# Kernel optimization log

Hardware: AMD Instinct MI355X
Metric: run time of the kernel (lower is better)

Reference implementation:

```python
import jax, jax.numpy as jnp
import numpy as np

N, E = 50000, 400000
IN_DIM = OUT_DIM = 128
T, R, H = 4, 8, 8
DK = OUT_DIM // H


def setup_inputs() -> dict:
    key = jax.random.key(0)
    ks = jax.random.split(key, 20)
    xav = lambda k, i, o: jax.random.uniform(k, (T, i, o), jnp.float32, -1.0, 1.0) * np.sqrt(6.0 / (i + o))
    return {
        "node_inp": jax.random.normal(ks[0], (N, IN_DIM), jnp.float32),
        "node_type": jax.random.randint(ks[1], (N,), 0, T),
        "edge_index": jax.random.randint(ks[2], (2, E), 0, N),
        "edge_type": jax.random.randint(ks[3], (E,), 0, R),
        "edge_sign": jax.random.randint(ks[4], (E,), 0, 3) - 1,  # values in {-1,0,1}
        "Wq": xav(ks[5], IN_DIM, OUT_DIM), "bq": jnp.zeros((T, OUT_DIM)),
        "Wk": xav(ks[6], IN_DIM, OUT_DIM), "bk": jnp.zeros((T, OUT_DIM)),
        "Wv": xav(ks[7], IN_DIM, OUT_DIM), "bv": jnp.zeros((T, OUT_DIM)),
        "rel_q": jax.random.normal(ks[8], (R, H, DK), jnp.float32),
        "rel_k": jax.random.normal(ks[9], (R, H, DK), jnp.float32),
        "rel_v": jax.random.normal(ks[10], (R, H, DK), jnp.float32),
        "sign_k_neutral": jnp.ones((H, DK), jnp.float32),
        "sign_v_neutral": jnp.ones((H, DK), jnp.float32),
        "rel_bias": jnp.zeros((R, H), jnp.float32),
        "skip": jnp.ones((T,), jnp.float32),
        "ln_gamma": jnp.ones((T, OUT_DIM), jnp.float32),
        "ln_beta": jnp.zeros((T, OUT_DIM), jnp.float32),
    }


def reference(node_inp, node_type, edge_index, edge_type, edge_sign,
              Wq, bq, Wk, bk, Wv, bv, rel_q, rel_k, rel_v,
              sign_k_neutral, sign_v_neutral, rel_bias, skip, ln_gamma, ln_beta):
    n = node_inp.shape[0]
    src, dst = edge_index[0], edge_index[1]
    rows = jnp.arange(n)
    # per-node-type linear projections: compute for all types, select by node_type
    proj = lambda W, b: (jnp.einsum('ni,tio->tno', node_inp, W) + b[:, None, :])[node_type, rows]
    Q = proj(Wq, bq).reshape(n, H, DK)
    K = proj(Wk, bk).reshape(n, H, DK)
    V = proj(Wv, bv).reshape(n, H, DK)
    # sign tables: [neg(-1), pos(+1), neutral]
    ones = jnp.ones((H, DK), node_inp.dtype)
    sign_k_all = jnp.stack([-ones, ones, sign_k_neutral], 0)
    sign_v_all = jnp.stack([-ones, ones, sign_v_neutral], 0)
    s_idx = jnp.where(edge_sign == -1, 0, jnp.where(edge_sign == 1, 1, 2))
    q_eff = Q[dst] * rel_q[edge_type]                      # [E,H,DK]
    k_eff = K[src] * rel_k[edge_type] * sign_k_all[s_idx]
    v_eff = V[src] * rel_v[edge_type] * sign_v_all[s_idx]
    scores = (q_eff * k_eff).sum(-1) / np.sqrt(DK) + rel_bias[edge_type]  # [E,H]
    # segment softmax over dst groups
    smax = jax.ops.segment_max(scores, dst, num_segments=n)
    ex = jnp.exp(scores - smax[dst])
    ssum = jax.ops.segment_sum(ex, dst, num_segments=n)
    attn = ex / (ssum[dst] + 1e-16)
    msg = (v_eff * attn[..., None]).reshape(-1, OUT_DIM)
    out = jnp.zeros((n, OUT_DIM), node_inp.dtype).at[dst].add(msg)
    # per-type gated skip + layernorm
    alpha = jax.nn.sigmoid(skip)[node_type][:, None]
    pre = alpha * out + (1.0 - alpha) * node_inp
    mu = pre.mean(-1, keepdims=True)
    var = ((pre - mu) ** 2).mean(-1, keepdims=True)
    normed = (pre - mu) / jnp.sqrt(var + 1e-5)
    return normed * ln_gamma[node_type] + ln_beta[node_type]
```

## Files before the change

### kernel.cpp

```cpp
#include <hip/hip_runtime.h>
#include <hip/hip_bf16.h>


#define D 128
#define NT 4
#define NR 8
#define NH 8
#define SCAN_BS 256

typedef unsigned short ushort_t;
typedef unsigned int uint_t;
typedef __attribute__((ext_vector_type(8))) short short8v;
typedef __attribute__((ext_vector_type(4))) float f32x4;

static __device__ __forceinline__ ushort_t f2bf(float f) {
    uint_t u = __float_as_uint(f);
    return (ushort_t)((u + 0x7FFFu + ((u >> 16) & 1u)) >> 16);
}
static __device__ __forceinline__ float bf2f(ushort_t h) {
    return __uint_as_float(((uint_t)h) << 16);
}

__global__ void k_hist(const int* __restrict__ nt, const int* __restrict__ ei,
                       int N, int E, int* __restrict__ tcnt, int* __restrict__ deg) {
    __shared__ int lcnt[NT];
    int tid = threadIdx.x;
    if (tid < NT) lcnt[tid] = 0;
    __syncthreads();
    int g = blockIdx.x * 256 + tid;
    if (g < N) atomicAdd(&lcnt[nt[g]], 1);
    if (g < E) atomicAdd(&deg[ei[E + g]], 1);
    __syncthreads();
    if (tid < NT && lcnt[tid]) atomicAdd(&tcnt[tid], lcnt[tid]);
}

__global__ __launch_bounds__(SCAN_BS) void k_scan1(const int* __restrict__ deg, int N,
                                                   int* __restrict__ bsum) {
    __shared__ int lds[SCAN_BS];
    int ti = threadIdx.x;
    int i = blockIdx.x * SCAN_BS + ti;
    lds[ti] = (i < N) ? deg[i] : 0;
    __syncthreads();
    for (int off = SCAN_BS >> 1; off > 0; off >>= 1) {
        if (ti < off) lds[ti] += lds[ti + off];
        __syncthreads();
    }
    if (ti == 0) bsum[blockIdx.x] = lds[0];
}

__global__ __launch_bounds__(SCAN_BS) void k_scan2(const int* __restrict__ bsum, int NB,
                                                   const int* __restrict__ tcnt,
                                                   int* __restrict__ bbase,
                                                   int* __restrict__ toff,
                                                   int* __restrict__ row_ptr, int N, int E) {
    __shared__ int lds[SCAN_BS];
    int ti = threadIdx.x;
    int v = (ti < NB) ? bsum[ti] : 0;
    lds[ti] = v;
    __syncthreads();
    for (int off = 1; off < SCAN_BS; off <<= 1) {
        int t = (ti >= off) ? lds[ti - off] : 0;
        __syncthreads();
        lds[ti] += t;
        __syncthreads();
    }
    if (ti < NB) bbase[ti] = lds[ti] - v;
    if (ti == 0) {
        int a = 0;
        for (int t = 0; t < NT; t++) { toff[t] = a; a += tcnt[t]; }
        toff[NT] = a;
        row_ptr[N] = E;
    }
}

__global__ __launch_bounds__(SCAN_BS) void k_scan3(const int* __restrict__ deg, int N,
                                                   const int* __restrict__ bbase,
                                                   int* __restrict__ row_ptr,
                                                   int* __restrict__ ecur) {
    __shared__ int lds[SCAN_BS];
    int ti = threadIdx.x;
    int i = blockIdx.x * SCAN_BS + ti;
    int v = (i < N) ? deg[i] : 0;
    lds[ti] = v;
    __syncthreads();
    for (int off = 1; off < SCAN_BS; off <<= 1) {
        int t = (ti >= off) ? lds[ti - off] : 0;
        __syncthreads();
        lds[ti] += t;
        __syncthreads();
    }
    if (i < N) {
        int ex = bbase[blockIdx.x] + lds[ti] - v;
        row_ptr[i] = ex;
        ecur[i] = ex;
    }
}

__global__ void k_scatter(const int* __restrict__ nt, const int* __restrict__ ei,
                          const int* __restrict__ et, const int* __restrict__ es,
                          int N, int E, int* __restrict__ tcur,
                          const int* __restrict__ toff, int* __restrict__ sorted,
                          int* __restrict__ ecur, int* __restrict__ csr_rec) {
    __shared__ int lcnt[NT];
    __shared__ int lbase[NT];
    int tid = threadIdx.x;
    if (tid < NT) lcnt[tid] = 0;
    __syncthreads();
    int g = blockIdx.x * 256 + tid;
    int t = -1, myrank = 0;
    if (g < N) {
        t = nt[g];
        myrank = atomicAdd(&lcnt[t], 1);
    }
    __syncthreads();
    if (tid < NT) lbase[tid] = lcnt[tid] ? atomicAdd(&tcur[tid], lcnt[tid]) : 0;
    __syncthreads();
    if (t >= 0) sorted[toff[t] + lbase[t] + myrank] = g;

    if (g < E) {
        int src = ei[g];
        int d = ei[E + g];
        int r = et[g];
        int sg = es[g];
        int p = atomicAdd(&ecur[d], 1);
        csr_rec[p] = src | (r << 17) | ((sg + 1) << 20);
    }
}

__global__ void k_wprep(const float* __restrict__ Wq, const float* __restrict__ Wk,
                        const float* __restrict__ Wv,
                        ushort_t* __restrict__ wt_hi, ushort_t* __restrict__ wt_lo) {
    int g = blockIdx.x * 256 + threadIdx.x;
    if (g >= 3 * NT * D * D) return;
    int o = g & 127;
    int k = (g >> 7) & 127;
    int t = (g >> 14) & 3;
    int m = g >> 16;
    const float* Wsel = (m == 0) ? Wq : (m == 1) ? Wk : Wv;
    float w = Wsel[((size_t)t * D + k) * D + o];
    ushort_t hi = f2bf(w);
    ushort_t lo = f2bf(w - bf2f(hi));
    size_t dst = (((size_t)(m * NT + t) * D) + o) * D + k;
    wt_hi[dst] = hi;
    wt_lo[dst] = lo;
}

__global__ void k_xprep(const float* __restrict__ x, const int* __restrict__ sorted,
                        int N, ushort_t* __restrict__ xs_hi, ushort_t* __restrict__ xs_lo) {
    int g = blockIdx.x * 256 + threadIdx.x;
    if (g >= N * 32) return;
    int i = g >> 5;
    int c4 = (g & 31) * 4;
    int node = sorted[i];
    float4 v = *(const float4*)(x + (size_t)node * D + c4);
    ushort4 h, l;
    h.x = f2bf(v.x); l.x = f2bf(v.x - bf2f(h.x));
    h.y = f2bf(v.y); l.y = f2bf(v.y - bf2f(h.y));
    h.z = f2bf(v.z); l.z = f2bf(v.z - bf2f(h.z));
    h.w = f2bf(v.w); l.w = f2bf(v.w - bf2f(h.w));
    *(ushort4*)(xs_hi + (size_t)i * D + c4) = h;
    *(ushort4*)(xs_lo + (size_t)i * D + c4) = l;
}

__global__ __launch_bounds__(512) void k_projm(
    const ushort_t* __restrict__ xs_hi, const ushort_t* __restrict__ xs_lo,
    const ushort_t* __restrict__ wt_hi, const ushort_t* __restrict__ wt_lo,
    const int* __restrict__ sorted, const int* __restrict__ toff,
    const float* __restrict__ bq, const float* __restrict__ bk,
    const float* __restrict__ bv,
    float* __restrict__ Q, ushort_t* __restrict__ Kb, ushort_t* __restrict__ Vb) {
    __shared__ int sid[128];
    int tid = threadIdx.x;
    int b = blockIdx.x;
    int t = -1, p0 = 0;
    int cum = 0;
    for (int tt = 0; tt < NT; tt++) {
        int cnt_t = toff[tt + 1] - toff[tt];
        int nb = (cnt_t + 127) >> 7;
        if (t < 0 && b < cum + nb) { t = tt; p0 = toff[tt] + (b - cum) * 128; }
        cum += nb;
    }
    if (t < 0) return;
    int tend = toff[t + 1];
    if (tid < 128) sid[tid] = (p0 + tid < tend) ? sorted[p0 + tid] : -1;
    __syncthreads();

    int w = tid >> 6, lane = tid & 63;
    int wr = w >> 2, wc = w & 3;
    int l15 = lane & 15, kq = lane >> 4;
    int m = blockIdx.y;

    const ushort_t* wth = wt_hi + ((size_t)(m * NT + t) * D) * D;
    const ushort_t* wtl = wt_lo + ((size_t)(m * NT + t) * D) * D;

    f32x4 acc[4][2];
#pragma unroll
    for (int fa = 0; fa < 4; fa++)
#pragma unroll
        for (int fb = 0; fb < 2; fb++) acc[fa][fb] = 0.f;

#pragma unroll
    for (int k0 = 0; k0 < D; k0 += 32) {
        int kk = k0 + kq * 8;
        short8v ah[4], al[4];
#pragma unroll
        for (int fa = 0; fa < 4; fa++) {
            size_t row = (size_t)(p0 + wr * 64 + fa * 16 + l15);
            ah[fa] = *(const short8v*)(xs_hi + row * D + kk);
            al[fa] = *(const short8v*)(xs_lo + row * D + kk);
        }
        short8v bh[2], bl[2];
#pragma unroll
        for (int fb = 0; fb < 2; fb++) {
            size_t col = (size_t)(wc * 32 + fb * 16 + l15);
            bh[fb] = *(const short8v*)(wth + col * D + kk);
            bl[fb] = *(const short8v*)(wtl + col * D + kk);
        }
#pragma unroll
        for (int fa = 0; fa < 4; fa++)
#pragma unroll
            for (int fb = 0; fb < 2; fb++) {
                acc[fa][fb] = __builtin_amdgcn_mfma_f32_16x16x32_bf16(
                    al[fa], bh[fb], acc[fa][fb], 0, 0, 0);
                acc[fa][fb] = __builtin_amdgcn_mfma_f32_16x16x32_bf16(
                    ah[fa], bl[fb], acc[fa][fb], 0, 0, 0);
                acc[fa][fb] = __builtin_amdgcn_mfma_f32_16x16x32_bf16(
                    ah[fa], bh[fb], acc[fa][fb], 0, 0, 0);
            }
    }

    const float* bm = (m == 0) ? bq : (m == 1) ? bk : bv;
    bm += t * D;
    float bias0 = bm[wc * 32 + l15];
    float bias1 = bm[wc * 32 + 16 + l15];
#pragma unroll
    for (int fa = 0; fa < 4; fa++) {
#pragma unroll
        for (int reg = 0; reg < 4; reg++) {
            int local = wr * 64 + fa * 16 + kq * 4 + reg;
            int node = sid[local];
            if (node < 0) continue;
            float v0 = acc[fa][0][reg] + bias0;
            float v1 = acc[fa][1][reg] + bias1;
            int col0 = wc * 32 + l15;
            if (m == 0) {
                Q[(size_t)node * D + col0] = v0;
                Q[(size_t)node * D + col0 + 16] = v1;
            } else {
                ushort_t* Om = (m == 1) ? Kb : Vb;
                Om[(size_t)node * D + col0] = f2bf(v0);
                Om[(size_t)node * D + col0 + 16] = f2bf(v1);
            }
        }
    }
}

__global__ __launch_bounds__(256) void k_agg(
    const int* __restrict__ row_ptr, const int* __restrict__ csr_rec,
    const int* __restrict__ nt, const float* __restrict__ x,
    const float* __restrict__ Qt, const ushort_t* __restrict__ Kb,
    const ushort_t* __restrict__ Vb, const float* __restrict__ rq,
    const float* __restrict__ rk, const float* __restrict__ rv,
    const float* __restrict__ skn, const float* __restrict__ svn,
    const float* __restrict__ rb, const float* __restrict__ skip,
    const float* __restrict__ gamma, const float* __restrict__ beta,
    float* __restrict__ out, int N) {
    __shared__ float l_rq[NR * 132];
    __shared__ float l_rk[NR * 132];
    __shared__ float l_rv[NR * 132];
    __shared__ float l_rb[NR * NH];
    int tid = threadIdx.x;
    for (int idx = tid; idx < NR * D; idx += 256) {
        int r = idx >> 7, c = idx & 127;
        l_rq[r * 132 + c] = rq[idx];
        l_rk[r * 132 + c] = rk[idx];
        l_rv[r * 132 + c] = rv[idx];
    }
    if (tid < NR * NH) l_rb[tid] = rb[tid];
    __syncthreads();

    int wid = (blockIdx.x * 256 + tid) >> 6;
    if (wid >= N) return;
    int lane = tid & 63;
    int h = lane >> 3, li = lane & 7;
    int d0 = lane * 2;
    int dst = wid;
    int rp0 = row_ptr[dst];
    int deg = row_ptr[dst + 1] - rp0;

    float4 q4[4], sk4[4];
#pragma unroll
    for (int j = 0; j < 4; j++) {
        q4[j] = *(const float4*)(Qt + (size_t)dst * D + h * 16 + 4 * j);
        sk4[j] = *(const float4*)(skn + h * 16 + 4 * j);
    }
    float2 sv2 = *(const float2*)(svn + d0);
    float2 xi = *(const float2*)(x + (size_t)dst * D + d0);
    int t = nt[dst];

    float m = -INFINITY, lsum = 0.f, acc0 = 0.f, acc1 = 0.f;

    for (int c0 = 0; c0 < deg; c0 += 8) {
        int cn = min(8, deg - c0);
        bool valid = li < cn;
        int recA = csr_rec[rp0 + c0 + (valid ? li : 0)];
        int srcA = recA & 0x1FFFF;
        int rA = (recA >> 17) & 7;
        int sgA = ((recA >> 20) & 3) - 1;
        bool neuA = (sgA == 0);
        float fsgA = (float)sgA;
        const ushort_t* kp = Kb + (size_t)srcA * D + h * 16;
        const float* rqp = &l_rq[rA * 132 + h * 16];
        const float* rkp = &l_rk[rA * 132 + h * 16];
        float dot = 0.f;
#pragma unroll
        for (int j = 0; j < 4; j++) {
            ushort4 kk = ((const ushort4*)kp)[j];
            float k0 = bf2f(kk.x), k1 = bf2f(kk.y), k2 = bf2f(kk.z), k3 = bf2f(kk.w);
            float4 a4 = *(const float4*)(rqp + 4 * j);
            float4 b4 = *(const float4*)(rkp + 4 * j);
            float f0 = neuA ? sk4[j].x : fsgA;
            float f1 = neuA ? sk4[j].y : fsgA;
            float f2 = neuA ? sk4[j].z : fsgA;
            float f3 = neuA ? sk4[j].w : fsgA;
            dot += q4[j].x * a4.x * k0 * b4.x * f0;
            dot += q4[j].y * a4.y * k1 * b4.y * f1;
            dot += q4[j].z * a4.z * k2 * b4.z * f2;
            dot += q4[j].w * a4.w * k3 * b4.w * f3;
        }
        float scA = valid ? dot * 0.25f + l_rb[rA * NH + h] : -INFINITY;
        float cm = scA;
        cm = fmaxf(cm, __shfl_xor(cm, 1));
        cm = fmaxf(cm, __shfl_xor(cm, 2));
        cm = fmaxf(cm, __shfl_xor(cm, 4));
        float nm = fmaxf(m, cm);
        float resc = __expf(m - nm);
        acc0 *= resc; acc1 *= resc; lsum *= resc;
        m = nm;
        int rec_[8];
        float w_[8];
        uint_t v2_[8];
#pragma unroll
        for (int i = 0; i < 8; i++) {
            rec_[i] = __shfl(recA, i);
            int src = rec_[i] & 0x1FFFF;
            v2_[i] = *(const uint_t*)(Vb + (size_t)src * D + d0);
            float s = __shfl(scA, (lane & 56) | i);
            w_[i] = __expf(s - m);
        }
#pragma unroll
        for (int i = 0; i < 8; i++) {
            float w = w_[i];
            lsum += w;
            int r = (rec_[i] >> 17) & 7;
            int sg = ((rec_[i] >> 20) & 3) - 1;
            float v0 = bf2f((ushort_t)(v2_[i] & 0xFFFF));
            float v1 = bf2f((ushort_t)(v2_[i] >> 16));
            float2 r2 = *(const float2*)(&l_rv[r * 132 + d0]);
            bool neu = (sg == 0);
            float f0 = neu ? sv2.x : (float)sg;
            float f1 = neu ? sv2.y : (float)sg;
            acc0 += w * v0 * r2.x * f0;
            acc1 += w * v1 * r2.y * f1;
        }
    }
    float winv = 1.f / (lsum + 1e-16f);
    float a0 = acc0 * winv, a1 = acc1 * winv;

    float alpha = 1.f / (1.f + __expf(-skip[t]));
    float p0 = alpha * a0 + (1.f - alpha) * xi.x;
    float p1 = alpha * a1 + (1.f - alpha) * xi.y;
    float rs = p0 + p1, rsq = p0 * p0 + p1 * p1;
#pragma unroll
    for (int o = 1; o < 64; o <<= 1) {
        rs += __shfl_xor(rs, o);
        rsq += __shfl_xor(rsq, o);
    }
    float mu = rs * (1.f / 128.f);
    float var = rsq * (1.f / 128.f) - mu * mu;
    float rstd = rsqrtf(var + 1e-5f);
    float2 g2 = *(const float2*)(gamma + t * D + d0);
    float2 b2 = *(const float2*)(beta + t * D + d0);
    float o0 = (p0 - mu) * rstd * g2.x + b2.x;
    float o1 = (p1 - mu) * rstd * g2.y + b2.y;
    *(float2*)(out + (size_t)dst * D + d0) = make_float2(o0, o1);
}

extern "C" void kernel_launch(void* const* d_in, const int* in_sizes, int n_in,
                              void* d_out, int out_size, void* d_ws, size_t ws_size,
                              hipStream_t stream) {
    const float* x   = (const float*)d_in[0];
    const int*  nt   = (const int*)d_in[1];
    const int*  ei   = (const int*)d_in[2];
    const int*  et   = (const int*)d_in[3];
    const int*  es   = (const int*)d_in[4];
    const float* Wq  = (const float*)d_in[5];
    const float* bq  = (const float*)d_in[6];
    const float* Wk  = (const float*)d_in[7];
    const float* bk  = (const float*)d_in[8];
    const float* Wv  = (const float*)d_in[9];
    const float* bv  = (const float*)d_in[10];
    const float* rq  = (const float*)d_in[11];
    const float* rk  = (const float*)d_in[12];
    const float* rv  = (const float*)d_in[13];
    const float* skn = (const float*)d_in[14];
    const float* svn = (const float*)d_in[15];
    const float* rb  = (const float*)d_in[16];
    const float* skp = (const float*)d_in[17];
    const float* gma = (const float*)d_in[18];
    const float* bta = (const float*)d_in[19];
    float* out = (float*)d_out;

    int N = in_sizes[0] / D;
    int E = in_sizes[2] / 2;
    int NB = (N + SCAN_BS - 1) / SCAN_BS;

    float*    Q     = (float*)d_ws;
    ushort_t* Kb    = (ushort_t*)(Q + (size_t)N * D);
    ushort_t* Vb    = Kb + (size_t)N * D;
    ushort_t* xs_hi = Vb + (size_t)N * D;
    ushort_t* xs_lo = xs_hi + (size_t)N * D;
    ushort_t* wt_hi = xs_lo + (size_t)N * D;
    ushort_t* wt_lo = wt_hi + (size_t)3 * NT * D * D;
    int* deg     = (int*)(wt_lo + (size_t)3 * NT * D * D);
    int* tcnt    = deg + N;
    int* tcur    = tcnt + NT;
    int* row_ptr = tcur + NT;
    int* ecur    = row_ptr + N + 1;
    int* toff    = ecur + N;
    int* sorted  = toff + 8;
    int* csr_rec = sorted + N;
    int* bsum    = csr_rec + E;
    int* bbase   = bsum + NB;

    hipMemsetAsync(deg, 0, (size_t)(N + 2 * NT) * sizeof(int), stream);

    int gbNE = (max(N, E) + 255) / 256;
    k_wprep<<<(3 * NT * D * D + 255) / 256, 256, 0, stream>>>(Wq, Wk, Wv, wt_hi, wt_lo);
    k_hist<<<gbNE, 256, 0, stream>>>(nt, ei, N, E, tcnt, deg);
    k_scan1<<<NB, SCAN_BS, 0, stream>>>(deg, N, bsum);
    k_scan2<<<1, SCAN_BS, 0, stream>>>(bsum, NB, tcnt, bbase, toff, row_ptr, N, E);
    k_scan3<<<NB, SCAN_BS, 0, stream>>>(deg, N, bbase, row_ptr, ecur);
    k_scatter<<<gbNE, 256, 0, stream>>>(nt, ei, et, es, N, E, tcur, toff, sorted,
                                        ecur, csr_rec);
    k_xprep<<<(N * 32 + 255) / 256, 256, 0, stream>>>(x, sorted, N, xs_hi, xs_lo);
    int nbp = (N + 127) / 128 + NT;
    k_projm<<<dim3(nbp, 3), 512, 0, stream>>>(xs_hi, xs_lo, wt_hi, wt_lo, sorted,
                                              toff, bq, bk, bv, Q, Kb, Vb);
    k_agg<<<(N * 64 + 255) / 256, 256, 0, stream>>>(row_ptr, csr_rec, nt, x, Q, Kb, Vb,
                                                    rq, rk, rv, skn, svn, rb, skp,
                                                    gma, bta, out, N);
}
```

Baseline: 330.1 us.

## Make aggregation kernel persistent with grid-stride waves and wider K loads

The aggregation kernel now launches a fixed grid of 2048 blocks in which each wave loops over destination nodes with a grid stride. The per-block LDS setup of relation tables is therefore amortised over many nodes instead of repeated in 12500 blocks. K rows are read as two 16-byte loads instead of four 8-byte ones, and each lane computes its own exponential once before it is shuffled, rather than every lane recomputing eight. A fixed grid can leave load imbalanced across waves when node degrees vary.

```diff
diff --git a/kernel.cpp b/kernel.cpp
--- a/kernel.cpp
+++ b/kernel.cpp
@@ -19,6 +19,12 @@
 }
 static __device__ __forceinline__ float bf2f(ushort_t h) {
     return __uint_as_float(((uint_t)h) << 16);
+}
+static __device__ __forceinline__ float bflo(uint_t u) {
+    return __uint_as_float(u << 16);
+}
+static __device__ __forceinline__ float bfhi(uint_t u) {
+    return __uint_as_float(u & 0xFFFF0000u);
 }
 
 __global__ void k_hist(const int* __restrict__ nt, const int* __restrict__ ei,
@@ -279,111 +285,123 @@
     if (tid < NR * NH) l_rb[tid] = rb[tid];
     __syncthreads();
 
-    int wid = (blockIdx.x * 256 + tid) >> 6;
-    if (wid >= N) return;
     int lane = tid & 63;
     int h = lane >> 3, li = lane & 7;
     int d0 = lane * 2;
-    int dst = wid;
-    int rp0 = row_ptr[dst];
-    int deg = row_ptr[dst + 1] - rp0;
-
-    float4 q4[4], sk4[4];
-#pragma unroll
-    for (int j = 0; j < 4; j++) {
-        q4[j] = *(const float4*)(Qt + (size_t)dst * D + h * 16 + 4 * j);
-        sk4[j] = *(const float4*)(skn + h * 16 + 4 * j);
-    }
+
+    float4 sk4[4];
+#pragma unroll
+    for (int j = 0; j < 4; j++) sk4[j] = *(const float4*)(skn + h * 16 + 4 * j);
     float2 sv2 = *(const float2*)(svn + d0);
-    float2 xi = *(const float2*)(x + (size_t)dst * D + d0);
-    int t = nt[dst];
-
-    float m = -INFINITY, lsum = 0.f, acc0 = 0.f, acc1 = 0.f;
-
-    for (int c0 = 0; c0 < deg; c0 += 8) {
-        int cn = min(8, deg - c0);
-        bool valid = li < cn;
-        int recA = csr_rec[rp0 + c0 + (valid ? li : 0)];
-        int srcA = recA & 0x1FFFF;
-        int rA = (recA >> 17) & 7;
-        int sgA = ((recA >> 20) & 3) - 1;
-        bool neuA = (sgA == 0);
-        float fsgA = (float)sgA;
-        const ushort_t* kp = Kb + (size_t)srcA * D + h * 16;
-        const float* rqp = &l_rq[rA * 132 + h * 16];
-        const float* rkp = &l_rk[rA * 132 + h * 16];
-        float dot = 0.f;
-#pragma unroll
-        for (int j = 0; j < 4; j++) {
-            ushort4 kk = ((const ushort4*)kp)[j];
-            float k0 = bf2f(kk.x), k1 = bf2f(kk.y), k2 = bf2f(kk.z), k3 = bf2f(kk.w);
-            float4 a4 = *(const float4*)(rqp + 4 * j);
-            float4 b4 = *(const float4*)(rkp + 4 * j);
-            float f0 = neuA ? sk4[j].x : fsgA;
-            float f1 = neuA ? sk4[j].y : fsgA;
-            float f2 = neuA ? sk4[j].z : fsgA;
-            float f3 = neuA ? sk4[j].w : fsgA;
-            dot += q4[j].x * a4.x * k0 * b4.x * f0;
-            dot += q4[j].y * a4.y * k1 * b4.y * f1;
-            dot += q4[j].z * a4.z * k2 * b4.z * f2;
-            dot += q4[j].w * a4.w * k3 * b4.w * f3;
+
+    int wid0 = (blockIdx.x * 256 + tid) >> 6;
+    int wstride = (gridDim.x * 256) >> 6;
+
+    for (int dst = wid0; dst < N; dst += wstride) {
+        int rp0 = row_ptr[dst];
+        int deg = row_ptr[dst + 1] - rp0;
+        float4 q4[4];
+#pragma unroll
+        for (int j = 0; j < 4; j++)
+            q4[j] = *(const float4*)(Qt + (size_t)dst * D + h * 16 + 4 * j);
+        float2 xi = *(const float2*)(x + (size_t)dst * D + d0);
+        int t = nt[dst];
+
+        float m = -INFINITY, lsum = 0.f, acc0 = 0.f, acc1 = 0.f;
+
+        for (int c0 = 0; c0 < deg; c0 += 8) {
+            int cn = min(8, deg - c0);
+            bool valid = li < cn;
+            int recA = csr_rec[rp0 + c0 + (valid ? li : 0)];
+            int srcA = recA & 0x1FFFF;
+            int rA = (recA >> 17) & 7;
+            int sgA = ((recA >> 20) & 3) - 1;
+            bool neuA = (sgA == 0);
+            float fsgA = (float)sgA;
+            const uint4* kp4 = (const uint4*)(Kb + (size_t)srcA * D + h * 16);
+            uint4 kA = kp4[0], kB = kp4[1];
+            float ke[16];
+            ke[0] = bflo(kA.x); ke[1] = bfhi(kA.x);
+            ke[2] = bflo(kA.y); ke[3] = bfhi(kA.y);
+            ke[4] = bflo(kA.z); ke[5] = bfhi(kA.z);
+            ke[6] = bflo(kA.w); ke[7] = bfhi(kA.w);
+            ke[8] = bflo(kB.x); ke[9] = bfhi(kB.x);
+            ke[10] = bflo(kB.y); ke[11] = bfhi(kB.y);
+            ke[12] = bflo(kB.z); ke[13] = bfhi(kB.z);
+            ke[14] = bflo(kB.w); ke[15] = bfhi(kB.w);
+            const float* rqp = &l_rq[rA * 132 + h * 16];
+            const float* rkp = &l_rk[rA * 132 + h * 16];
+            float dot = 0.f;
+#pragma unroll
+            for (int j = 0; j < 4; j++) {
+                float4 a4 = *(const float4*)(rqp + 4 * j);
+                float4 b4 = *(const float4*)(rkp + 4 * j);
+                float f0 = neuA ? sk4[j].x : fsgA;
+                float f1 = neuA ? sk4[j].y : fsgA;
+                float f2 = neuA ? sk4[j].z : fsgA;
+                float f3 = neuA ? sk4[j].w : fsgA;
+                dot += q4[j].x * a4.x * ke[4 * j] * b4.x * f0;
+                dot += q4[j].y * a4.y * ke[4 * j + 1] * b4.y * f1;
+                dot += q4[j].z * a4.z * ke[4 * j + 2] * b4.z * f2;
+                dot += q4[j].w * a4.w * ke[4 * j + 3] * b4.w * f3;
+            }
+            float scA = valid ? dot * 0.25f + l_rb[rA * NH + h] : -INFINITY;
+            float cm = scA;
+            cm = fmaxf(cm, __shfl_xor(cm, 1));
+            cm = fmaxf(cm, __shfl_xor(cm, 2));
+            cm = fmaxf(cm, __shfl_xor(cm, 4));
+            float nm = fmaxf(m, cm);
+            float resc = __expf(m - nm);
+            acc0 *= resc; acc1 *= resc; lsum *= resc;
+            m = nm;
+            float expA = __expf(scA - m);
+            int rec_[8];
+            float w_[8];
+            uint_t v2_[8];
+#pragma unroll
+            for (int i = 0; i < 8; i++) {
+                rec_[i] = __shfl(recA, i);
+                int src = rec_[i] & 0x1FFFF;
+                v2_[i] = *(const uint_t*)(Vb + (size_t)src * D + d0);
+                w_[i] = __shfl(expA, (lane & 56) | i);
+            }
+#pragma unroll
+            for (int i = 0; i < 8; i++) {
+                float w = w_[i];
+                lsum += w;
+                int r = (rec_[i] >> 17) & 7;
+                int sg = ((rec_[i] >> 20) & 3) - 1;
+                float v0 = bflo(v2_[i]);
+                float v1 = bfhi(v2_[i]);
+                float2 r2 = *(const float2*)(&l_rv[r * 132 + d0]);
+                bool neu = (sg == 0);
+                float f0 = neu ? sv2.x : (float)sg;
+                float f1 = neu ? sv2.y : (float)sg;
+                acc0 += w * v0 * r2.x * f0;
+                acc1 += w * v1 * r2.y * f1;
+            }
         }
-        float scA = valid ? dot * 0.25f + l_rb[rA * NH + h] : -INFINITY;
-        float cm = scA;
-        cm = fmaxf(cm, __shfl_xor(cm, 1));
-        cm = fmaxf(cm, __shfl_xor(cm, 2));
-        cm = fmaxf(cm, __shfl_xor(cm, 4));
-        float nm = fmaxf(m, cm);
-        float resc = __expf(m - nm);
-        acc0 *= resc; acc1 *= resc; lsum *= resc;
-        m = nm;
-        int rec_[8];
-        float w_[8];
-        uint_t v2_[8];
-#pragma unroll
-        for (int i = 0; i < 8; i++) {
-            rec_[i] = __shfl(recA, i);
-            int src = rec_[i] & 0x1FFFF;
-            v2_[i] = *(const uint_t*)(Vb + (size_t)src * D + d0);
-            float s = __shfl(scA, (lane & 56) | i);
-            w_[i] = __expf(s - m);
+        float winv = 1.f / (lsum + 1e-16f);
+        float a0 = acc0 * winv, a1 = acc1 * winv;
+
+        float alpha = 1.f / (1.f + __expf(-skip[t]));
+        float p0 = alpha * a0 + (1.f - alpha) * xi.x;
+        float p1 = alpha * a1 + (1.f - alpha) * xi.y;
+        float rs = p0 + p1, rsq = p0 * p0 + p1 * p1;
+#pragma unroll
+        for (int o = 1; o < 64; o <<= 1) {
+            rs += __shfl_xor(rs, o);
+            rsq += __shfl_xor(rsq, o);
         }
-#pragma unroll
-        for (int i = 0; i < 8; i++) {
-            float w = w_[i];
-            lsum += w;
-            int r = (rec_[i] >> 17) & 7;
-            int sg = ((rec_[i] >> 20) & 3) - 1;
-            float v0 = bf2f((ushort_t)(v2_[i] & 0xFFFF));
-            float v1 = bf2f((ushort_t)(v2_[i] >> 16));
-            float2 r2 = *(const float2*)(&l_rv[r * 132 + d0]);
-            bool neu = (sg == 0);
-            float f0 = neu ? sv2.x : (float)sg;
-            float f1 = neu ? sv2.y : (float)sg;
-            acc0 += w * v0 * r2.x * f0;
-            acc1 += w * v1 * r2.y * f1;
-        }
-    }
-    float winv = 1.f / (lsum + 1e-16f);
-    float a0 = acc0 * winv, a1 = acc1 * winv;
-
-    float alpha = 1.f / (1.f + __expf(-skip[t]));
-    float p0 = alpha * a0 + (1.f - alpha) * xi.x;
-    float p1 = alpha * a1 + (1.f - alpha) * xi.y;
-    float rs = p0 + p1, rsq = p0 * p0 + p1 * p1;
-#pragma unroll
-    for (int o = 1; o < 64; o <<= 1) {
-        rs += __shfl_xor(rs, o);
-        rsq += __shfl_xor(rsq, o);
-    }
-    float mu = rs * (1.f / 128.f);
-    float var = rsq * (1.f / 128.f) - mu * mu;
-    float rstd = rsqrtf(var + 1e-5f);
-    float2 g2 = *(const float2*)(gamma + t * D + d0);
-    float2 b2 = *(const float2*)(beta + t * D + d0);
-    float o0 = (p0 - mu) * rstd * g2.x + b2.x;
-    float o1 = (p1 - mu) * rstd * g2.y + b2.y;
-    *(float2*)(out + (size_t)dst * D + d0) = make_float2(o0, o1);
+        float mu = rs * (1.f / 128.f);
+        float var = rsq * (1.f / 128.f) - mu * mu;
+        float rstd = rsqrtf(var + 1e-5f);
+        float2 g2 = *(const float2*)(gamma + t * D + d0);
+        float2 b2 = *(const float2*)(beta + t * D + d0);
+        float o0 = (p0 - mu) * rstd * g2.x + b2.x;
+        float o1 = (p1 - mu) * rstd * g2.y + b2.y;
+        *(float2*)(out + (size_t)dst * D + d0) = make_float2(o0, o1);
+    }
 }
 
 extern "C" void kernel_launch(void* const* d_in, const int* in_sizes, int n_in,
@@ -447,7 +465,7 @@
     int nbp = (N + 127) / 128 + NT;
     k_projm<<<dim3(nbp, 3), 512, 0, stream>>>(xs_hi, xs_lo, wt_hi, wt_lo, sorted,
                                               toff, bq, bk, bv, Q, Kb, Vb);
-    k_agg<<<(N * 64 + 255) / 256, 256, 0, stream>>>(row_ptr, csr_rec, nt, x, Q, Kb, Vb,
-                                                    rq, rk, rv, skn, svn, rb, skp,
-                                                    gma, bta, out, N);
-}
+    k_agg<<<2048, 256, 0, stream>>>(row_ptr, csr_rec, nt, x, Q, Kb, Vb,
+                                    rq, rk, rv, skn, svn, rb, skp,
+                                    gma, bta, out, N);
+}
```

Result: faster. 310.5 us (-5.9%).
